# Performance work log

Measured on AMD Instinct MI355X. Metric: run time of the kernel, lower is better.

Reference implementation:

```python
import jax, jax.numpy as jnp
import numpy as np
from jax import lax

B, N, D, S, K = 8, 4096, 61, 1024, 32
MLP = (64, 64, 128)
WN = (3, 8, 8, 16)  # WeightNet: 3 -> 8 -> 8 -> 16
EPS = 1e-5


def _gather(p, idx):
    # p: [B, N, C], idx: [B, ...] -> [B, ..., C]
    return jax.vmap(lambda pb, ib: pb[ib])(p, idx)


def _fps(xyz, npoint, key):
    # farthest point sampling, xyz: [B, N, 3] -> idx [B, npoint]
    b, n, _ = xyz.shape
    start = jax.random.randint(key, (b,), 0, n)
    def step(carry, _):
        dmin, far = carry
        centroid = jnp.take_along_axis(xyz, far[:, None, None], axis=1)  # [B,1,3]
        d = jnp.sum((xyz - centroid) ** 2, -1)                            # [B,N]
        dmin = jnp.minimum(dmin, d)
        return (dmin, jnp.argmax(dmin, -1)), far
    _, idxs = lax.scan(step, (jnp.full((b, n), 1e10, xyz.dtype), start), None, length=npoint)
    return idxs.T  # [B, npoint]


def _sqdist(a, b):
    # a: [B,S,3], b: [B,N,3] -> [B,S,N]
    return (jnp.sum(a ** 2, -1)[:, :, None] + jnp.sum(b ** 2, -1)[:, None, :]
            - 2.0 * jnp.einsum('bsc,bnc->bsn', a, b))


def _bn_relu(x, g, be):
    # channels-last BN (training-mode batch stats, biased var) + ReLU
    axes = tuple(range(x.ndim - 1))
    m = x.mean(axes, keepdims=True)
    v = x.var(axes, keepdims=True)
    return jax.nn.relu(g * (x - m) * lax.rsqrt(v + EPS) + be)


def _forward(xyz, points, mlp_p, wn_p, lin_w, lin_b, bnl_g, bnl_b):
    xyz_t = xyz.transpose(0, 2, 1)    # [B,N,3]
    pts = points.transpose(0, 2, 1)   # [B,N,D]
    xyz_sg = lax.stop_gradient(xyz_t)  # index computations carry no grads (as in torch)
    fps_idx = _fps(xyz_sg, S, jax.random.key(42))  # [B,S]
    new_xyz = _gather(xyz_t, fps_idx)              # [B,S,3]
    idx = lax.top_k(-_sqdist(lax.stop_gradient(new_xyz), xyz_sg), K)[1]  # [B,S,K]
    g_norm = _gather(xyz_t, idx) - new_xyz[:, :, None, :]                # [B,S,K,3]
    feat = jnp.concatenate([g_norm, _gather(pts, idx)], -1)              # [B,S,K,3+D]
    for w, b, g, be in mlp_p:
        feat = _bn_relu(jnp.einsum('bskc,oc->bsko', feat, w) + b, g, be)
    wts = g_norm
    for w, b, g, be in wn_p:
        wts = _bn_relu(jnp.einsum('bskc,oc->bsko', wts, w) + b, g, be)   # [B,S,K,16]
    # [B,S,C,K] @ [B,S,K,16] -> [B,S,C,16] -> [B,S,C*16] (C-major flatten, as torch .view)
    agg = jnp.einsum('bskc,bskw->bscw', feat, wts).reshape(B, S, -1)
    out = agg @ lin_w.T + lin_b                                          # [B,S,128]
    m = out.mean((0, 1), keepdims=True)  # BatchNorm1d over batch and spatial
    v = out.var((0, 1), keepdims=True)
    out = jax.nn.relu(bnl_g * (out - m) * lax.rsqrt(v + EPS) + bnl_b)
    return new_xyz.transpose(0, 2, 1), out.transpose(0, 2, 1)  # [B,3,S], [B,128,S]


def setup_inputs() -> dict:
    key = jax.random.key(0)
    ks = iter(jax.random.split(key, 64))
    inp = {"xyz": jax.random.normal(next(ks), (B, 3, N), jnp.float32),
           "points": jax.random.normal(next(ks), (B, D, N), jnp.float32)}
    mlp_in = (3 + D,) + MLP[:-1]
    for i, (ci, co) in enumerate(zip(mlp_in, MLP)):
        inp[f"mlp_w{i}"] = jax.random.normal(next(ks), (co, ci), jnp.float32) / np.float32(np.sqrt(ci))
        inp[f"mlp_b{i}"] = jnp.zeros((co,), jnp.float32)
        inp[f"mlp_g{i}"] = jnp.ones((co,), jnp.float32)
        inp[f"mlp_be{i}"] = jnp.zeros((co,), jnp.float32)
    for i, (ci, co) in enumerate(zip(WN[:-1], WN[1:])):
        inp[f"wn_w{i}"] = jax.random.normal(next(ks), (co, ci), jnp.float32) / np.float32(np.sqrt(ci))
        inp[f"wn_b{i}"] = jnp.zeros((co,), jnp.float32)
        inp[f"wn_g{i}"] = jnp.ones((co,), jnp.float32)
        inp[f"wn_be{i}"] = jnp.zeros((co,), jnp.float32)
    fin = 16 * MLP[-1]
    inp["lin_w"] = jax.random.normal(next(ks), (MLP[-1], fin), jnp.float32) / np.float32(np.sqrt(fin))
    inp["lin_b"] = jnp.zeros((MLP[-1],), jnp.float32)
    inp["bnl_g"] = jnp.ones((MLP[-1],), jnp.float32)
    inp["bnl_b"] = jnp.zeros((MLP[-1],), jnp.float32)
    return inp


def reference(xyz, points, mlp_w0, mlp_b0, mlp_g0, mlp_be0, mlp_w1, mlp_b1, mlp_g1, mlp_be1, mlp_w2, mlp_b2, mlp_g2, mlp_be2, wn_w0, wn_b0, wn_g0, wn_be0, wn_w1, wn_b1, wn_g1, wn_be1, wn_w2, wn_b2, wn_g2, wn_be2, lin_w, lin_b, bnl_g, bnl_b):
    mlp_p = [(mlp_w0, mlp_b0, mlp_g0, mlp_be0),
             (mlp_w1, mlp_b1, mlp_g1, mlp_be1),
             (mlp_w2, mlp_b2, mlp_g2, mlp_be2)]
    wn_p = [(wn_w0, wn_b0, wn_g0, wn_be0),
            (wn_w1, wn_b1, wn_g1, wn_be1),
            (wn_w2, wn_b2, wn_g2, wn_be2)]
    return _forward(xyz, points, mlp_p, wn_p, lin_w, lin_b, bnl_g, bnl_b)
```

## Files before the change

kernel.cpp:

```cpp
#include <hip/hip_runtime.h>
#include <cstdint>
#include <cstddef>


constexpr int B_ = 8, N_ = 4096, D_ = 61, S_ = 1024, K_ = 32;
constexpr int P_ = B_ * S_ * K_;
constexpr int BS_ = B_ * S_;

constexpr size_t OFF_STATS  = 0;
constexpr size_t OFF_NEWXYZ = 8192;
constexpr size_t OFF_KNN    = 106496;
constexpr size_t OFF_PT     = 1155072;
constexpr size_t OFF_Y01    = 9543680;
constexpr size_t OFF_Y2     = 76652544;
constexpr size_t OFF_W01    = 210870272;
constexpr size_t OFF_W2B    = 219258880;
constexpr size_t OFF_OUTPRE = OFF_W01;

static inline uint32_t rotl32(uint32_t x, int r){ return (x << r) | (x >> (32 - r)); }
static void tf2x32(uint32_t k0, uint32_t k1, uint32_t x0, uint32_t x1,
                   uint32_t* o0, uint32_t* o1){
  uint32_t ks[3] = {k0, k1, k0 ^ k1 ^ 0x1BD11BDAu};
  x0 += ks[0]; x1 += ks[1];
  const int RA[4] = {13,15,26,6}, RB[4] = {17,29,16,24};
  for (int i = 0; i < 5; ++i){
    const int* R = (i & 1) ? RB : RA;
    for (int j = 0; j < 4; ++j){ x0 += x1; x1 = rotl32(x1, R[j]); x1 ^= x0; }
    x0 += ks[(i+1)%3]; x1 += ks[(i+2)%3] + (uint32_t)(i+1);
  }
  *o0 = x0; *o1 = x1;
}
struct StartIdx { int v[8]; };
static StartIdx compute_starts(){
  uint32_t ka, kb;
  tf2x32(0u, 42u, 0u, 1u, &ka, &kb);
  StartIdx s;
  for (int i = 0; i < 8; ++i){
    uint32_t b1, b2;
    tf2x32(ka, kb, 0u, (uint32_t)i, &b1, &b2);
    s.v[i] = (int)((b1 ^ b2) & 4095u);
  }
  return s;
}

template<int C>
__device__ __forceinline__ float dpp_max_f32_step(float x){
  int t = __builtin_amdgcn_update_dpp(0, (int)__float_as_uint(x), C, 0xf, 0xf, true);
  return fmaxf(x, __uint_as_float((unsigned)t));
}
__device__ __forceinline__ float dpp_wave_max_f32(float x){
  x = dpp_max_f32_step<0x111>(x);
  x = dpp_max_f32_step<0x112>(x);
  x = dpp_max_f32_step<0x114>(x);
  x = dpp_max_f32_step<0x118>(x);
  x = dpp_max_f32_step<0x142>(x);
  x = dpp_max_f32_step<0x143>(x);
  return __uint_as_float((unsigned)__builtin_amdgcn_readlane((int)__float_as_uint(x), 63));
}
template<int C>
__device__ __forceinline__ unsigned dpp_min_u32_step(unsigned x){
  int t = __builtin_amdgcn_update_dpp(-1, (int)x, C, 0xf, 0xf, false);
  unsigned u = (unsigned)t;
  return u < x ? u : x;
}
__device__ __forceinline__ unsigned dpp_wave_min_u32(unsigned x){
  x = dpp_min_u32_step<0x111>(x);
  x = dpp_min_u32_step<0x112>(x);
  x = dpp_min_u32_step<0x114>(x);
  x = dpp_min_u32_step<0x118>(x);
  x = dpp_min_u32_step<0x142>(x);
  x = dpp_min_u32_step<0x143>(x);
  return (unsigned)__builtin_amdgcn_readlane((int)x, 63);
}
template<int C>
__device__ __forceinline__ unsigned long long dpp_min_u64_step(unsigned long long k){
  unsigned lo = (unsigned)k, hi = (unsigned)(k >> 32);
  unsigned olo = (unsigned)__builtin_amdgcn_update_dpp(-1, (int)lo, C, 0xf, 0xf, false);
  unsigned ohi = (unsigned)__builtin_amdgcn_update_dpp(-1, (int)hi, C, 0xf, 0xf, false);
  unsigned long long o = ((unsigned long long)ohi << 32) | olo;
  return o < k ? o : k;
}
__device__ __forceinline__ unsigned long long dpp_wave_min_u64(unsigned long long k){
  k = dpp_min_u64_step<0x111>(k);
  k = dpp_min_u64_step<0x112>(k);
  k = dpp_min_u64_step<0x114>(k);
  k = dpp_min_u64_step<0x118>(k);
  k = dpp_min_u64_step<0x142>(k);
  k = dpp_min_u64_step<0x143>(k);
  unsigned lo = (unsigned)__builtin_amdgcn_readlane((int)(unsigned)k, 63);
  unsigned hi = (unsigned)__builtin_amdgcn_readlane((int)(unsigned)(k >> 32), 63);
  return ((unsigned long long)hi << 32) | lo;
}
__device__ __forceinline__ unsigned ordf(float f){
  unsigned u = __float_as_uint(f);
  return u ^ (unsigned)(((int)u >> 31) | 0x80000000);
}

__global__ __launch_bounds__(64) void tr_kernel(const float* __restrict__ pts,
                                                float* __restrict__ pT){
  __shared__ float tile[61][65];
  const int b = blockIdx.x >> 6;
  const int n0 = (blockIdx.x & 63) * 64;
  const int t = threadIdx.x;
  for (int d = 0; d < 61; ++d)
    tile[d][t] = pts[((size_t)b*61 + d)*N_ + n0 + t];
  __syncthreads();
  for (int r = 0; r < 64; ++r)
    pT[((size_t)b*N_ + n0 + r)*64 + t] = (t < 61) ? tile[t][r] : 0.f;
}

#define REP8(M) M(0) M(1) M(2) M(3) M(4) M(5) M(6) M(7)

__global__ __launch_bounds__(512, 1) void fps_kernel(const float* __restrict__ xyz,
                                                     StartIdx st,
                                                     float* __restrict__ new_xyz,
                                                     float* __restrict__ out_xyz){
  const int b = blockIdx.x, tid = threadIdx.x;
  const int lane = tid & 63, wv = tid >> 6;
  const float* xb = xyz + (size_t)b*3*N_;
  __shared__ float4 pts4[N_];
  __shared__ unsigned long long slots[2][8];

#define LOADP(i) \
  float px##i = xb[tid + 512*(i)]; \
  float py##i = xb[N_ + tid + 512*(i)]; \
  float pz##i = xb[2*N_ + tid + 512*(i)]; \
  float dm##i = 1e10f; \
  pts4[tid + 512*(i)] = make_float4(px##i, py##i, pz##i, 0.f);
  REP8(LOADP)
#undef LOADP
  __syncthreads();

  const int start = st.v[b];
  float4 c4 = pts4[start];
  float cx = c4.x, cy = c4.y, cz = c4.z;

  int par = 0;
  for (int s = 0; s < S_; ++s){
    if (tid == 0){
      new_xyz[((size_t)b*S_ + s)*3 + 0] = cx;
      new_xyz[((size_t)b*S_ + s)*3 + 1] = cy;
      new_xyz[((size_t)b*S_ + s)*3 + 2] = cz;
      out_xyz[(size_t)b*3*S_ + s]        = cx;
      out_xyz[(size_t)b*3*S_ + S_ + s]   = cy;
      out_xyz[(size_t)b*3*S_ + 2*S_ + s] = cz;
    }
#define UPD(i) { \
      float dx = __fsub_rn(px##i, cx), dy = __fsub_rn(py##i, cy), dz = __fsub_rn(pz##i, cz); \
      float d  = __fadd_rn(__fadd_rn(__fmul_rn(dx,dx), __fmul_rn(dy,dy)), __fmul_rn(dz,dz)); \
      dm##i = fminf(dm##i, d); }
    REP8(UPD)
#undef UPD
    float m01 = fmaxf(dm0, dm1), m23 = fmaxf(dm2, dm3);
    float m45 = fmaxf(dm4, dm5), m67 = fmaxf(dm6, dm7);
    float lmax = fmaxf(fmaxf(m01, m23), fmaxf(m45, m67));
    float wmax = dpp_wave_max_f32(lmax);
    unsigned cand = 0xFFFFFFFFu;
#define CAND(i) cand = (dm##i == wmax) ? (unsigned)(tid + 512*(i)) : cand;
    CAND(7) CAND(6) CAND(5) CAND(4) CAND(3) CAND(2) CAND(1) CAND(0)
#undef CAND
    unsigned widx = dpp_wave_min_u32(cand);
    if (lane == 63)
      slots[par][wv] = ((unsigned long long)__float_as_uint(wmax) << 32)
                     | (unsigned long long)(unsigned)(~widx);
    __syncthreads();
    unsigned long long bk = slots[par][0];
    { unsigned long long v1 = slots[par][1]; if (v1 > bk) bk = v1;
      unsigned long long v2 = slots[par][2]; if (v2 > bk) bk = v2;
      unsigned long long v3 = slots[par][3]; if (v3 > bk) bk = v3;
      unsigned long long v4 = slots[par][4]; if (v4 > bk) bk = v4;
      unsigned long long v5 = slots[par][5]; if (v5 > bk) bk = v5;
      unsigned long long v6 = slots[par][6]; if (v6 > bk) bk = v6;
      unsigned long long v7 = slots[par][7]; if (v7 > bk) bk = v7; }
    const int winner = (int)(~(unsigned)bk) & (N_ - 1);
    float4 w4 = pts4[winner];
    cx = w4.x; cy = w4.y; cz = w4.z;
    par ^= 1;
  }
}
#undef REP8

__global__ __launch_bounds__(256) void knn_kernel(const float* __restrict__ xyz,
                                                  const float* __restrict__ nxyz,
                                                  int* __restrict__ knn_idx){
  __shared__ float dist[4][4096];
  const int wv = threadIdx.x >> 6, lane = threadIdx.x & 63;
  const int q = blockIdx.x*4 + wv;
  const int b = q >> 10;
  const float* xb = xyz + (size_t)b*3*N_;
  const float ax = nxyz[(size_t)q*3], ay = nxyz[(size_t)q*3+1], az = nxyz[(size_t)q*3+2];
  const float sa = __fadd_rn(__fadd_rn(__fmul_rn(ax,ax), __fmul_rn(ay,ay)), __fmul_rn(az,az));
  float* dw = dist[wv];
  unsigned long long kk = ~0ull;
  for (int i = 0; i < 64; ++i){
    int n = i*64 + lane;
    float x = xb[n], y = xb[N_+n], z = xb[2*N_+n];
    float sb  = __fadd_rn(__fadd_rn(__fmul_rn(x,x), __fmul_rn(y,y)), __fmul_rn(z,z));
    float dot = __fadd_rn(__fadd_rn(__fmul_rn(ax,x), __fmul_rn(ay,y)), __fmul_rn(az,z));
    float d   = __fsub_rn(__fadd_rn(sa, sb), __fmul_rn(2.f, dot));
    dw[i*64 + ((lane + i) & 63)] = d;
    unsigned long long key = ((unsigned long long)ordf(d) << 32) | (unsigned)n;
    if (key < kk) kk = key;
  }
  __syncthreads();
  int myout = 0;
  for (int r = 0; r < 32; ++r){
    unsigned long long g = dpp_wave_min_u64(kk);
    const int gn = (int)(g & 0xFFFFFFFFull);
    if (lane == r) myout = gn;
    const int col = gn & 63, row = gn >> 6;
    const int a = lane*64 + ((col + lane) & 63);
    float v = dw[a];
    if (lane == row){ v = 3.4e38f; dw[a] = 3.4e38f; }
    unsigned long long nk = ((unsigned long long)ordf(v) << 32)
                          | (unsigned)(lane*64 + col);
    nk = dpp_wave_min_u64(nk);
    if (lane == col) kk = nk;
  }
  if (lane < 32) knn_idx[(size_t)q*32 + lane] = myout;
}

__global__ __launch_bounds__(256, 2) void m0_kernel(const float* __restrict__ pT,
                                                    const float* __restrict__ xyz,
                                                    const float* __restrict__ nxyz,
                                                    const int* __restrict__ knn_idx,
                                                    const float* __restrict__ w,
                                                    const float* __restrict__ bias,
                                                    float* __restrict__ y){
  __shared__ float Wt[4096]; __shared__ float bb[64];
  for (int t = threadIdx.x; t < 4096; t += 256){ int o = t >> 6, c = t & 63; Wt[c*64+o] = w[o*64+c]; }
  if (threadIdx.x < 64) bb[threadIdx.x] = bias[threadIdx.x];
  __syncthreads();
  const int p = blockIdx.x*256 + threadIdx.x;
  const int b = p >> 15, s = (p & 32767) >> 5;
  const int n = knn_idx[p];
  float in[64];
  {
    const float* xb = xyz + (size_t)b*3*N_;
    const int q = (b << 10) + s;
    in[0] = xb[n]       - nxyz[(size_t)q*3];
    in[1] = xb[N_+n]    - nxyz[(size_t)q*3+1];
    in[2] = xb[2*N_+n]  - nxyz[(size_t)q*3+2];
    const float* pr = pT + ((size_t)b*N_ + n)*64;
#pragma unroll
    for (int d = 0; d < 60; d += 4){
      float4 v = *reinterpret_cast<const float4*>(&pr[d]);
      in[3+d] = v.x; in[4+d] = v.y; in[5+d] = v.z; in[6+d] = v.w;
    }
    in[63] = pr[60];
  }
  float acc[64];
#pragma unroll
  for (int o = 0; o < 64; ++o) acc[o] = bb[o];
#pragma unroll
  for (int c = 0; c < 64; ++c){
    float x = in[c];
#pragma unroll
    for (int o = 0; o < 64; o += 4){
      float4 w4 = *reinterpret_cast<const float4*>(&Wt[c*64+o]);
      acc[o]   += x*w4.x; acc[o+1] += x*w4.y; acc[o+2] += x*w4.z; acc[o+3] += x*w4.w;
    }
  }
#pragma unroll
  for (int o = 0; o < 64; ++o) y[(size_t)o*P_ + p] = acc[o];
}

__global__ __launch_bounds__(256) void stats_kernel(const float* __restrict__ y,
                                                    double* __restrict__ st, int C){
  const int c = blockIdx.x % C, chunk = blockIdx.x / C;
  const float4* row4 = reinterpret_cast<const float4*>(y + (size_t)c*P_ + (size_t)chunk*32768);
  double s = 0.0, q = 0.0;
  for (int i = threadIdx.x; i < 8192; i += 256){
    float4 v = row4[i];
    s += (double)v.x + (double)v.y + (double)v.z + (double)v.w;
    q += (double)v.x*v.x + (double)v.y*v.y + (double)v.z*v.z + (double)v.w*v.w;
  }
  __shared__ double ss[256], qq[256];
  ss[threadIdx.x] = s; qq[threadIdx.x] = q; __syncthreads();
  for (int w = 128; w >= 1; w >>= 1){
    if (threadIdx.x < w){ ss[threadIdx.x] += ss[threadIdx.x+w]; qq[threadIdx.x] += qq[threadIdx.x+w]; }
    __syncthreads();
  }
  if (threadIdx.x == 0){ atomicAdd(&st[c*2], ss[0]); atomicAdd(&st[c*2+1], qq[0]); }
}

__device__ __forceinline__ void bn_coeff(const double* st, const float* g, const float* be,
                                         int c, double cnt, float* sc, float* sh){
  double mean = st[c*2] / cnt;
  double var  = st[c*2+1] / cnt - mean*mean;
  double scale = (double)g[c] / sqrt(var + 1e-5);
  *sc = (float)scale; *sh = (float)((double)be[c] - mean*scale);
}

__global__ __launch_bounds__(256, 2) void m1_kernel(float* __restrict__ y,
                                                    const float* __restrict__ w,
                                                    const float* __restrict__ bias,
                                                    const double* __restrict__ st,
                                                    const float* __restrict__ g,
                                                    const float* __restrict__ be){
  __shared__ float Wt[4096]; __shared__ float bb[64], sc[64], sh[64];
  for (int t = threadIdx.x; t < 4096; t += 256){ int o = t >> 6, c = t & 63; Wt[c*64+o] = w[o*64+c]; }
  if (threadIdx.x < 64){
    bn_coeff(st, g, be, threadIdx.x, (double)P_, &sc[threadIdx.x], &sh[threadIdx.x]);
    bb[threadIdx.x] = bias[threadIdx.x];
  }
  __syncthreads();
  const int p = blockIdx.x*256 + threadIdx.x;
  float in[64];
#pragma unroll
  for (int c = 0; c < 64; ++c){
    float x = y[(size_t)c*P_ + p];
    in[c] = fmaxf(0.f, fmaf(x, sc[c], sh[c]));
  }
  float acc[64];
#pragma unroll
  for (int o = 0; o < 64; ++o) acc[o] = bb[o];
#pragma unroll
  for (int c = 0; c < 64; ++c){
    float x = in[c];
#pragma unroll
    for (int o = 0; o < 64; o += 4){
      float4 w4 = *reinterpret_cast<const float4*>(&Wt[c*64+o]);
      acc[o]   += x*w4.x; acc[o+1] += x*w4.y; acc[o+2] += x*w4.z; acc[o+3] += x*w4.w;
    }
  }
#pragma unroll
  for (int o = 0; o < 64; ++o) y[(size_t)o*P_ + p] = acc[o];
}

__global__ __launch_bounds__(256, 2) void m2_kernel(const float* __restrict__ y1,
                                                    float* __restrict__ y2,
                                                    const float* __restrict__ w,
                                                    const float* __restrict__ bias,
                                                    const double* __restrict__ st,
                                                    const float* __restrict__ g,
                                                    const float* __restrict__ be){
  __shared__ float Wt[4096]; __shared__ float bb[64], sc[64], sh[64];
  const int half = blockIdx.y;
  for (int t = threadIdx.x; t < 4096; t += 256){
    int o = t >> 6, c = t & 63;
    Wt[c*64+o] = w[(size_t)(half*64+o)*64 + c];
  }
  if (threadIdx.x < 64){
    bn_coeff(st, g, be, threadIdx.x, (double)P_, &sc[threadIdx.x], &sh[threadIdx.x]);
    bb[threadIdx.x] = bias[half*64 + threadIdx.x];
  }
  __syncthreads();
  const int p = blockIdx.x*256 + threadIdx.x;
  float in[64];
#pragma unroll
  for (int c = 0; c < 64; ++c){
    float x = y1[(size_t)c*P_ + p];
    in[c] = fmaxf(0.f, fmaf(x, sc[c], sh[c]));
  }
  float acc[64];
#pragma unroll
  for (int o = 0; o < 64; ++o) acc[o] = bb[o];
#pragma unroll
  for (int c = 0; c < 64; ++c){
    float x = in[c];
#pragma unroll
    for (int o = 0; o < 64; o += 4){
      float4 w4 = *reinterpret_cast<const float4*>(&Wt[c*64+o]);
      acc[o]   += x*w4.x; acc[o+1] += x*w4.y; acc[o+2] += x*w4.z; acc[o+3] += x*w4.w;
    }
  }
#pragma unroll
  for (int o = 0; o < 64; ++o) y2[(size_t)(half*64+o)*P_ + p] = acc[o];
}

__global__ __launch_bounds__(256) void w0_kernel(const float* __restrict__ xyz,
                                                 const float* __restrict__ nxyz,
                                                 const int* __restrict__ knn_idx,
                                                 const float* __restrict__ w,
                                                 const float* __restrict__ bias,
                                                 float* __restrict__ wb){
  __shared__ float Wl[24], bb[8];
  if (threadIdx.x < 24) Wl[threadIdx.x] = w[threadIdx.x];
  if (threadIdx.x < 8)  bb[threadIdx.x] = bias[threadIdx.x];
  __syncthreads();
  const int p = blockIdx.x*256 + threadIdx.x;
  const int b = p >> 15, s = (p & 32767) >> 5;
  const int n = knn_idx[p];
  const float* xb = xyz + (size_t)b*3*N_;
  const int q = (b << 10) + s;
  float gx = xb[n]      - nxyz[(size_t)q*3];
  float gy = xb[N_+n]   - nxyz[(size_t)q*3+1];
  float gz = xb[2*N_+n] - nxyz[(size_t)q*3+2];
#pragma unroll
  for (int o = 0; o < 8; ++o){
    float a = bb[o] + gx*Wl[o*3] + gy*Wl[o*3+1] + gz*Wl[o*3+2];
    wb[(size_t)o*P_ + p] = a;
  }
}

__global__ __launch_bounds__(256) void w1_kernel(float* __restrict__ wb,
                                                 const float* __restrict__ w,
                                                 const float* __restrict__ bias,
                                                 const double* __restrict__ st,
                                                 const float* __restrict__ g,
                                                 const float* __restrict__ be){
  __shared__ float Wl[64], bb[8], sc[8], sh[8];
  if (threadIdx.x < 64) Wl[threadIdx.x] = w[threadIdx.x];
  if (threadIdx.x < 8){
    bn_coeff(st, g, be, threadIdx.x, (double)P_, &sc[threadIdx.x], &sh[threadIdx.x]);
    bb[threadIdx.x] = bias[threadIdx.x];
  }
  __syncthreads();
  const int p = blockIdx.x*256 + threadIdx.x;
  float in[8];
#pragma unroll
  for (int c = 0; c < 8; ++c){
    float x = wb[(size_t)c*P_ + p];
    in[c] = fmaxf(0.f, fmaf(x, sc[c], sh[c]));
  }
  float acc[8];
#pragma unroll
  for (int o = 0; o < 8; ++o){
    float a = bb[o];
#pragma unroll
    for (int c = 0; c < 8; ++c) a += in[c]*Wl[o*8+c];
    acc[o] = a;
  }
#pragma unroll
  for (int o = 0; o < 8; ++o) wb[(size_t)o*P_ + p] = acc[o];
}

__global__ __launch_bounds__(256) void w2_kernel(const float* __restrict__ wb,
                                                 float* __restrict__ wb2,
                                                 const float* __restrict__ w,
                                                 const float* __restrict__ bias,
                                                 const double* __restrict__ st,
                                                 const float* __restrict__ g,
                                                 const float* __restrict__ be){
  __shared__ float Wl[128], bb[16], sc[8], sh[8];
  if (threadIdx.x < 128) Wl[threadIdx.x] = w[threadIdx.x];
  if (threadIdx.x < 8)
    bn_coeff(st, g, be, threadIdx.x, (double)P_, &sc[threadIdx.x], &sh[threadIdx.x]);
  if (threadIdx.x < 16) bb[threadIdx.x] = bias[threadIdx.x];
  __syncthreads();
  const int p = blockIdx.x*256 + threadIdx.x;
  float in[8];
#pragma unroll
  for (int c = 0; c < 8; ++c){
    float x = wb[(size_t)c*P_ + p];
    in[c] = fmaxf(0.f, fmaf(x, sc[c], sh[c]));
  }
#pragma unroll
  for (int o = 0; o < 16; ++o){
    float a = bb[o];
#pragma unroll
    for (int c = 0; c < 8; ++c) a += in[c]*Wl[o*8+c];
    wb2[(size_t)o*P_ + p] = a;
  }
}

__global__ __launch_bounds__(256) void agg_kernel(const float* __restrict__ y2,
                                                  const float* __restrict__ wb2,
                                                  const double* __restrict__ st2,
                                                  const float* __restrict__ g2,
                                                  const float* __restrict__ be2,
                                                  const double* __restrict__ stw,
                                                  const float* __restrict__ gw,
                                                  const float* __restrict__ bew,
                                                  float* __restrict__ agg){
  __shared__ float f[32*132];
  __shared__ float wt[32*16];
  __shared__ float sc2[128], sh2[128], scw[16], shw[16];
  const int t = threadIdx.x;
  if (t < 128) bn_coeff(st2, g2, be2, t, (double)P_, &sc2[t], &sh2[t]);
  if (t < 16)  bn_coeff(stw, gw, bew, t, (double)P_, &scw[t], &shw[t]);
  __syncthreads();
  const int bs = blockIdx.x;
  const size_t p0 = (size_t)bs * 32;
  for (int e = t; e < 4096; e += 256){
    int c = e >> 5, k = e & 31;
    float x = y2[(size_t)c*P_ + p0 + k];
    f[k*132 + c] = fmaxf(0.f, fmaf(x, sc2[c], sh2[c]));
  }
  for (int e = t; e < 512; e += 256){
    int w = e >> 5, k = e & 31;
    float x = wb2[(size_t)w*P_ + p0 + k];
    wt[k*16 + w] = fmaxf(0.f, fmaf(x, scw[w], shw[w]));
  }
  __syncthreads();
  const int c = t >> 1, wp = (t & 1) * 8;
  float a0=0,a1=0,a2=0,a3=0,a4=0,a5=0,a6=0,a7=0;
#pragma unroll
  for (int k = 0; k < 32; ++k){
    float fv = f[k*132 + c];
    float4 u = *reinterpret_cast<const float4*>(&wt[k*16 + wp]);
    float4 v = *reinterpret_cast<const float4*>(&wt[k*16 + wp + 4]);
    a0 += fv*u.x; a1 += fv*u.y; a2 += fv*u.z; a3 += fv*u.w;
    a4 += fv*v.x; a5 += fv*v.y; a6 += fv*v.z; a7 += fv*v.w;
  }
  float* dst = agg + (size_t)bs*2048 + c*16 + wp;
  *reinterpret_cast<float4*>(dst)     = make_float4(a0,a1,a2,a3);
  *reinterpret_cast<float4*>(dst + 4) = make_float4(a4,a5,a6,a7);
}

__global__ __launch_bounds__(256) void lin_kernel(const float* __restrict__ agg,
                                                  const float* __restrict__ lw,
                                                  const float* __restrict__ lb,
                                                  float* __restrict__ outp){
  __shared__ float A[32*33];
  __shared__ float Wl[32*128];
  __shared__ float lbs[128];
  const int t = threadIdx.x;
  const int r0 = blockIdx.x * 32;
  if (t < 128) lbs[t] = lb[t];
  const int c_lane = t & 31, rg = t >> 5;
  float acc[4][4];
#pragma unroll
  for (int i = 0; i < 4; ++i)
#pragma unroll
    for (int j = 0; j < 4; ++j) acc[i][j] = 0.f;

  for (int kk0 = 0; kk0 < 2048; kk0 += 32){
    __syncthreads();
    {
      int r = t >> 3, kq = (t & 7) * 4;
      float4 v = *reinterpret_cast<const float4*>(&agg[(size_t)(r0 + r)*2048 + kk0 + kq]);
      A[r*33 + kq]   = v.x; A[r*33 + kq+1] = v.y; A[r*33 + kq+2] = v.z; A[r*33 + kq+3] = v.w;
    }
    {
#pragma unroll
      for (int u = 0; u < 4; ++u){
        int fid = t + 256*u;
        int o = fid >> 3, kq = (fid & 7) * 4;
        float4 v = *reinterpret_cast<const float4*>(&lw[(size_t)o*2048 + kk0 + kq]);
        Wl[(kq  )*128 + o] = v.x; Wl[(kq+1)*128 + o] = v.y;
        Wl[(kq+2)*128 + o] = v.z; Wl[(kq+3)*128 + o] = v.w;
      }
    }
    __syncthreads();
#pragma unroll 8
    for (int kk = 0; kk < 32; ++kk){
      float a0 = A[(rg*4+0)*33 + kk], a1 = A[(rg*4+1)*33 + kk],
            a2 = A[(rg*4+2)*33 + kk], a3 = A[(rg*4+3)*33 + kk];
#pragma unroll
      for (int j = 0; j < 4; ++j){
        float wv = Wl[kk*128 + c_lane + 32*j];
        acc[0][j] += a0*wv; acc[1][j] += a1*wv; acc[2][j] += a2*wv; acc[3][j] += a3*wv;
      }
    }
  }
  __syncthreads();
#pragma unroll
  for (int i = 0; i < 4; ++i)
#pragma unroll
    for (int j = 0; j < 4; ++j){
      int o = c_lane + 32*j;
      outp[(size_t)(r0 + rg*4 + i)*128 + o] = acc[i][j] + lbs[o];
    }
}

__global__ __launch_bounds__(128) void statsF_kernel(const float* __restrict__ outp,
                                                     double* __restrict__ st){
  const int c = threadIdx.x;
  const int r0 = blockIdx.x * 128;
  double s = 0.0, q = 0.0;
  for (int r = 0; r < 128; ++r){
    double v = outp[(size_t)(r0 + r)*128 + c];
    s += v; q += v*v;
  }
  atomicAdd(&st[c*2], s); atomicAdd(&st[c*2+1], q);
}

__global__ __launch_bounds__(256) void final_kernel(const float* __restrict__ outp,
                                                    const double* __restrict__ st,
                                                    const float* __restrict__ g,
                                                    const float* __restrict__ be,
                                                    float* __restrict__ out){
  const int gid = blockIdx.x*256 + threadIdx.x;
  const int s = gid & 1023, o = (gid >> 10) & 127, b = gid >> 17;
  float sc, sh;
  bn_coeff(st, g, be, o, (double)BS_, &sc, &sh);
  float x = outp[((size_t)(b << 10) + s)*128 + o];
  out[gid] = fmaxf(0.f, fmaf(x, sc, sh));
}

extern "C" void kernel_launch(void* const* d_in, const int* in_sizes, int n_in,
                              void* d_out, int out_size, void* d_ws, size_t ws_size,
                              hipStream_t stream){
  (void)in_sizes; (void)n_in; (void)out_size; (void)ws_size;
  const float* xyz    = (const float*)d_in[0];
  const float* points = (const float*)d_in[1];
  const float* mw0 = (const float*)d_in[2],  *mb0 = (const float*)d_in[3],
             * mg0 = (const float*)d_in[4],  *me0 = (const float*)d_in[5];
  const float* mw1 = (const float*)d_in[6],  *mb1 = (const float*)d_in[7],
             * mg1 = (const float*)d_in[8],  *me1 = (const float*)d_in[9];
  const float* mw2 = (const float*)d_in[10], *mb2 = (const float*)d_in[11],
             * mg2 = (const float*)d_in[12], *me2 = (const float*)d_in[13];
  const float* ww0 = (const float*)d_in[14], *wb0 = (const float*)d_in[15],
             * wg0 = (const float*)d_in[16], *we0 = (const float*)d_in[17];
  const float* ww1 = (const float*)d_in[18], *wb1 = (const float*)d_in[19],
             * wg1 = (const float*)d_in[20], *we1 = (const float*)d_in[21];
  const float* ww2 = (const float*)d_in[22], *wb2_ = (const float*)d_in[23],
             * wg2 = (const float*)d_in[24], *we2 = (const float*)d_in[25];
  const float* lw  = (const float*)d_in[26], *lb  = (const float*)d_in[27];
  const float* fg  = (const float*)d_in[28], *fb  = (const float*)d_in[29];

  char* ws = (char*)d_ws;
  double* ST0 = (double*)(ws + OFF_STATS);
  double* ST1 = (double*)(ws + OFF_STATS + 1024);
  double* ST2 = (double*)(ws + OFF_STATS + 2048);
  double* SW0 = (double*)(ws + OFF_STATS + 4096);
  double* SW1 = (double*)(ws + OFF_STATS + 4224);
  double* SW2 = (double*)(ws + OFF_STATS + 4352);
  double* STF = (double*)(ws + OFF_STATS + 4608);
  float* nxyz   = (float*)(ws + OFF_NEWXYZ);
  int*   knnidx = (int*)(ws + OFF_KNN);
  float* pT     = (float*)(ws + OFF_PT);
  float* y01    = (float*)(ws + OFF_Y01);
  float* y2     = (float*)(ws + OFF_Y2);
  float* w01    = (float*)(ws + OFF_W01);
  float* w2b    = (float*)(ws + OFF_W2B);
  float* aggbuf = (float*)(ws + OFF_Y01);
  float* outpre = (float*)(ws + OFF_OUTPRE);

  float* out_xyz  = (float*)d_out;
  float* out_feat = (float*)d_out + (size_t)B_*3*S_;

  hipMemsetAsync(ws + OFF_STATS, 0, 8192, stream);

  tr_kernel<<<dim3(B_*64), dim3(64), 0, stream>>>(points, pT);

  StartIdx st = compute_starts();
  fps_kernel<<<dim3(B_), dim3(512), 0, stream>>>(xyz, st, nxyz, out_xyz);

  knn_kernel<<<dim3(BS_/4), dim3(256), 0, stream>>>(xyz, nxyz, knnidx);

  m0_kernel<<<dim3(P_/256), dim3(256), 0, stream>>>(pT, xyz, nxyz, knnidx, mw0, mb0, y01);
  stats_kernel<<<dim3(64*8), dim3(256), 0, stream>>>(y01, ST0, 64);
  m1_kernel<<<dim3(P_/256), dim3(256), 0, stream>>>(y01, mw1, mb1, ST0, mg0, me0);
  stats_kernel<<<dim3(64*8), dim3(256), 0, stream>>>(y01, ST1, 64);
  m2_kernel<<<dim3(P_/256, 2), dim3(256), 0, stream>>>(y01, y2, mw2, mb2, ST1, mg1, me1);
  stats_kernel<<<dim3(128*8), dim3(256), 0, stream>>>(y2, ST2, 128);

  w0_kernel<<<dim3(P_/256), dim3(256), 0, stream>>>(xyz, nxyz, knnidx, ww0, wb0, w01);
  stats_kernel<<<dim3(8*8), dim3(256), 0, stream>>>(w01, SW0, 8);
  w1_kernel<<<dim3(P_/256), dim3(256), 0, stream>>>(w01, ww1, wb1, SW0, wg0, we0);
  stats_kernel<<<dim3(8*8), dim3(256), 0, stream>>>(w01, SW1, 8);
  w2_kernel<<<dim3(P_/256), dim3(256), 0, stream>>>(w01, w2b, ww2, wb2_, SW1, wg1, we1);
  stats_kernel<<<dim3(16*8), dim3(256), 0, stream>>>(w2b, SW2, 16);

  agg_kernel<<<dim3(BS_), dim3(256), 0, stream>>>(y2, w2b, ST2, mg2, me2, SW2, wg2, we2, aggbuf);
  lin_kernel<<<dim3(BS_/32), dim3(256), 0, stream>>>(aggbuf, lw, lb, outpre);
  statsF_kernel<<<dim3(BS_/128), dim3(128), 0, stream>>>(outpre, STF);
  final_kernel<<<dim3((B_*128*S_)/256), dim3(256), 0, stream>>>(outpre, STF, fg, fb, out_feat);
}
```

Measured before the change: 1.558 ms.

## Fuse BN stats into producer kernels, merge transpose into FPS, streamline FPS argmax

Removes the six standalone stats kernels by computing per-channel sum and sum-of-squares inside each producer kernel, using DPP row reductions, shared memory and double atomics. This saves re-reading the large activation buffers. The points transpose now runs as extra blocks of the FPS launch so it overlaps the single-block-per-batch FPS. FPS uses one packed 64-bit key max-reduction and defers writing the sampled coordinates until after the loop. The final kernel transposes through shared memory for coalesced stores. Stats are now accumulated in fp32 within a block before the double atomics, which slightly changes numerics, and the added atomics may contend.

```diff
diff --git a/kernel.cpp b/kernel.cpp
--- a/kernel.cpp
+++ b/kernel.cpp
@@ -44,33 +44,21 @@
 }
 
 template<int C>
-__device__ __forceinline__ float dpp_max_f32_step(float x){
-  int t = __builtin_amdgcn_update_dpp(0, (int)__float_as_uint(x), C, 0xf, 0xf, true);
-  return fmaxf(x, __uint_as_float((unsigned)t));
-}
-__device__ __forceinline__ float dpp_wave_max_f32(float x){
-  x = dpp_max_f32_step<0x111>(x);
-  x = dpp_max_f32_step<0x112>(x);
-  x = dpp_max_f32_step<0x114>(x);
-  x = dpp_max_f32_step<0x118>(x);
-  x = dpp_max_f32_step<0x142>(x);
-  x = dpp_max_f32_step<0x143>(x);
-  return __uint_as_float((unsigned)__builtin_amdgcn_readlane((int)__float_as_uint(x), 63));
-}
-template<int C>
-__device__ __forceinline__ unsigned dpp_min_u32_step(unsigned x){
-  int t = __builtin_amdgcn_update_dpp(-1, (int)x, C, 0xf, 0xf, false);
-  unsigned u = (unsigned)t;
-  return u < x ? u : x;
-}
-__device__ __forceinline__ unsigned dpp_wave_min_u32(unsigned x){
-  x = dpp_min_u32_step<0x111>(x);
-  x = dpp_min_u32_step<0x112>(x);
-  x = dpp_min_u32_step<0x114>(x);
-  x = dpp_min_u32_step<0x118>(x);
-  x = dpp_min_u32_step<0x142>(x);
-  x = dpp_min_u32_step<0x143>(x);
-  return (unsigned)__builtin_amdgcn_readlane((int)x, 63);
+__device__ __forceinline__ unsigned long long dpp_max_u64_step(unsigned long long k){
+  unsigned lo = (unsigned)k, hi = (unsigned)(k >> 32);
+  unsigned olo = (unsigned)__builtin_amdgcn_update_dpp(0, (int)lo, C, 0xf, 0xf, true);
+  unsigned ohi = (unsigned)__builtin_amdgcn_update_dpp(0, (int)hi, C, 0xf, 0xf, true);
+  unsigned long long o = ((unsigned long long)ohi << 32) | olo;
+  return o > k ? o : k;
+}
+__device__ __forceinline__ unsigned long long dpp_wave_max_u64(unsigned long long k){
+  k = dpp_max_u64_step<0x111>(k);
+  k = dpp_max_u64_step<0x112>(k);
+  k = dpp_max_u64_step<0x114>(k);
+  k = dpp_max_u64_step<0x118>(k);
+  k = dpp_max_u64_step<0x142>(k);
+  k = dpp_max_u64_step<0x143>(k);
+  return k;
 }
 template<int C>
 __device__ __forceinline__ unsigned long long dpp_min_u64_step(unsigned long long k){
@@ -91,78 +79,95 @@
   unsigned hi = (unsigned)__builtin_amdgcn_readlane((int)(unsigned)(k >> 32), 63);
   return ((unsigned long long)hi << 32) | lo;
 }
+template<int C>
+__device__ __forceinline__ float dpp_add_step(float x){
+  int t = __builtin_amdgcn_update_dpp(0, (int)__float_as_uint(x), C, 0xf, 0xf, true);
+  return x + __uint_as_float((unsigned)t);
+}
+__device__ __forceinline__ float dpp_row_sum16(float x){
+  x = dpp_add_step<0x111>(x);
+  x = dpp_add_step<0x112>(x);
+  x = dpp_add_step<0x114>(x);
+  x = dpp_add_step<0x118>(x);
+  return x;
+}
 __device__ __forceinline__ unsigned ordf(float f){
   unsigned u = __float_as_uint(f);
   return u ^ (unsigned)(((int)u >> 31) | 0x80000000);
 }
-
-__global__ __launch_bounds__(64) void tr_kernel(const float* __restrict__ pts,
-                                                float* __restrict__ pT){
-  __shared__ float tile[61][65];
-  const int b = blockIdx.x >> 6;
-  const int n0 = (blockIdx.x & 63) * 64;
-  const int t = threadIdx.x;
-  for (int d = 0; d < 61; ++d)
-    tile[d][t] = pts[((size_t)b*61 + d)*N_ + n0 + t];
-  __syncthreads();
-  for (int r = 0; r < 64; ++r)
-    pT[((size_t)b*N_ + n0 + r)*64 + t] = (t < 61) ? tile[t][r] : 0.f;
+__device__ __forceinline__ void atomAddD(double* p, double v){
+  __hip_atomic_fetch_add(p, v, __ATOMIC_RELAXED, __HIP_MEMORY_SCOPE_AGENT);
 }
 
 #define REP8(M) M(0) M(1) M(2) M(3) M(4) M(5) M(6) M(7)
 
-__global__ __launch_bounds__(512, 1) void fps_kernel(const float* __restrict__ xyz,
-                                                     StartIdx st,
-                                                     float* __restrict__ new_xyz,
-                                                     float* __restrict__ out_xyz){
-  const int b = blockIdx.x, tid = threadIdx.x;
+__global__ __launch_bounds__(512, 1) void fps_tr_kernel(const float* __restrict__ xyz,
+                                                        const float* __restrict__ pts,
+                                                        StartIdx st,
+                                                        float* __restrict__ new_xyz,
+                                                        float* __restrict__ out_xyz,
+                                                        float* __restrict__ pT){
+  __shared__ float4 pts4[N_];
+  __shared__ unsigned short win[S_];
+  __shared__ unsigned long long slots[2][8];
+  const int tid = threadIdx.x;
+
+  if (blockIdx.x >= 8){
+    float* tile = (float*)pts4;
+    const int tt = blockIdx.x - 8;
+    const int b = tt >> 6, n0 = (tt & 63) * 64;
+    for (int e = tid; e < 61*64; e += 512){
+      int d = e >> 6, c = e & 63;
+      tile[d*65 + c] = pts[((size_t)b*61 + d)*N_ + n0 + c];
+    }
+    __syncthreads();
+    for (int e = tid; e < 4096; e += 512){
+      int r = e >> 6, d = e & 63;
+      pT[((size_t)b*N_ + n0 + r)*64 + d] = (d < 61) ? tile[d*65 + r] : 0.f;
+    }
+    return;
+  }
+
+  const int b = blockIdx.x;
   const int lane = tid & 63, wv = tid >> 6;
   const float* xb = xyz + (size_t)b*3*N_;
-  __shared__ float4 pts4[N_];
-  __shared__ unsigned long long slots[2][8];
 
 #define LOADP(i) \
   float px##i = xb[tid + 512*(i)]; \
   float py##i = xb[N_ + tid + 512*(i)]; \
   float pz##i = xb[2*N_ + tid + 512*(i)]; \
   float dm##i = 1e10f; \
+  const unsigned kl##i = ~(unsigned)(tid + 512*(i)); \
   pts4[tid + 512*(i)] = make_float4(px##i, py##i, pz##i, 0.f);
   REP8(LOADP)
 #undef LOADP
   __syncthreads();
 
-  const int start = st.v[b];
-  float4 c4 = pts4[start];
+  int cur = st.v[b];
+  float4 c4 = pts4[cur];
   float cx = c4.x, cy = c4.y, cz = c4.z;
 
   int par = 0;
   for (int s = 0; s < S_; ++s){
-    if (tid == 0){
-      new_xyz[((size_t)b*S_ + s)*3 + 0] = cx;
-      new_xyz[((size_t)b*S_ + s)*3 + 1] = cy;
-      new_xyz[((size_t)b*S_ + s)*3 + 2] = cz;
-      out_xyz[(size_t)b*3*S_ + s]        = cx;
-      out_xyz[(size_t)b*3*S_ + S_ + s]   = cy;
-      out_xyz[(size_t)b*3*S_ + 2*S_ + s] = cz;
-    }
-#define UPD(i) { \
+    if (tid == 0) win[s] = (unsigned short)cur;
+    if (s == S_ - 1) break;
+#define UPD(i) \
+    unsigned long long key##i; { \
       float dx = __fsub_rn(px##i, cx), dy = __fsub_rn(py##i, cy), dz = __fsub_rn(pz##i, cz); \
       float d  = __fadd_rn(__fadd_rn(__fmul_rn(dx,dx), __fmul_rn(dy,dy)), __fmul_rn(dz,dz)); \
-      dm##i = fminf(dm##i, d); }
+      dm##i = fminf(dm##i, d); \
+      key##i = ((unsigned long long)__float_as_uint(dm##i) << 32) | kl##i; }
     REP8(UPD)
 #undef UPD
-    float m01 = fmaxf(dm0, dm1), m23 = fmaxf(dm2, dm3);
-    float m45 = fmaxf(dm4, dm5), m67 = fmaxf(dm6, dm7);
-    float lmax = fmaxf(fmaxf(m01, m23), fmaxf(m45, m67));
-    float wmax = dpp_wave_max_f32(lmax);
-    unsigned cand = 0xFFFFFFFFu;
-#define CAND(i) cand = (dm##i == wmax) ? (unsigned)(tid + 512*(i)) : cand;
-    CAND(7) CAND(6) CAND(5) CAND(4) CAND(3) CAND(2) CAND(1) CAND(0)
-#undef CAND
-    unsigned widx = dpp_wave_min_u32(cand);
-    if (lane == 63)
-      slots[par][wv] = ((unsigned long long)__float_as_uint(wmax) << 32)
-                     | (unsigned long long)(unsigned)(~widx);
+    unsigned long long t0 = key0 > key1 ? key0 : key1;
+    unsigned long long t1 = key2 > key3 ? key2 : key3;
+    unsigned long long t2 = key4 > key5 ? key4 : key5;
+    unsigned long long t3 = key6 > key7 ? key6 : key7;
+    unsigned long long u0 = t0 > t1 ? t0 : t1;
+    unsigned long long u1 = t2 > t3 ? t2 : t3;
+    unsigned long long k  = u0 > u1 ? u0 : u1;
+    k = dpp_wave_max_u64(k);
+    if (lane == 63) slots[par][wv] = k;
     __syncthreads();
     unsigned long long bk = slots[par][0];
     { unsigned long long v1 = slots[par][1]; if (v1 > bk) bk = v1;
@@ -172,10 +177,20 @@
       unsigned long long v5 = slots[par][5]; if (v5 > bk) bk = v5;
       unsigned long long v6 = slots[par][6]; if (v6 > bk) bk = v6;
       unsigned long long v7 = slots[par][7]; if (v7 > bk) bk = v7; }
-    const int winner = (int)(~(unsigned)bk) & (N_ - 1);
-    float4 w4 = pts4[winner];
+    cur = (int)(~(unsigned)bk) & (N_ - 1);
+    float4 w4 = pts4[cur];
     cx = w4.x; cy = w4.y; cz = w4.z;
     par ^= 1;
+  }
+  __syncthreads();
+  for (int s2 = tid; s2 < S_; s2 += 512){
+    float4 p = pts4[win[s2]];
+    new_xyz[((size_t)b*S_ + s2)*3 + 0] = p.x;
+    new_xyz[((size_t)b*S_ + s2)*3 + 1] = p.y;
+    new_xyz[((size_t)b*S_ + s2)*3 + 2] = p.z;
+    out_xyz[(size_t)b*3*S_ + s2]        = p.x;
+    out_xyz[(size_t)b*3*S_ + S_ + s2]   = p.y;
+    out_xyz[(size_t)b*3*S_ + 2*S_ + s2] = p.z;
   }
 }
 #undef REP8
@@ -220,14 +235,51 @@
   if (lane < 32) knn_idx[(size_t)q*32 + lane] = myout;
 }
 
+__device__ __forceinline__ void bn_coeff(const double* st, const float* g, const float* be,
+                                         int c, double cnt, float* sc, float* sh){
+  double mean = st[c*2] / cnt;
+  double var  = st[c*2+1] / cnt - mean*mean;
+  double scale = (double)g[c] / sqrt(var + 1e-5);
+  *sc = (float)scale; *sh = (float)((double)be[c] - mean*scale);
+}
+
+#define STATS64(ACC_EXPR, ST, CH_OFF)                                          \
+  {                                                                            \
+    _Pragma("unroll")                                                          \
+    for (int o = 0; o < 64; ++o){                                              \
+      float v_ = (ACC_EXPR);                                                   \
+      float s1_ = dpp_row_sum16(v_);                                           \
+      float q1_ = dpp_row_sum16(v_*v_);                                        \
+      if ((threadIdx.x & 15) == 15){                                           \
+        int rid_ = threadIdx.x >> 4;                                           \
+        redS[rid_][o] = s1_; redQ[rid_][o] = q1_;                              \
+      }                                                                        \
+    }                                                                          \
+    __syncthreads();                                                           \
+    if (threadIdx.x < 64){                                                     \
+      float s_ = 0.f;                                                          \
+      _Pragma("unroll")                                                        \
+      for (int r_ = 0; r_ < 16; ++r_) s_ += redS[r_][threadIdx.x];             \
+      atomAddD(&(ST)[((CH_OFF) + threadIdx.x)*2], (double)s_);                 \
+    } else if (threadIdx.x < 128){                                             \
+      int o_ = threadIdx.x - 64;                                               \
+      float s_ = 0.f;                                                          \
+      _Pragma("unroll")                                                        \
+      for (int r_ = 0; r_ < 16; ++r_) s_ += redQ[r_][o_];                      \
+      atomAddD(&(ST)[((CH_OFF) + o_)*2 + 1], (double)s_);                      \
+    }                                                                          \
+  }
+
 __global__ __launch_bounds__(256, 2) void m0_kernel(const float* __restrict__ pT,
                                                     const float* __restrict__ xyz,
                                                     const float* __restrict__ nxyz,
                                                     const int* __restrict__ knn_idx,
                                                     const float* __restrict__ w,
                                                     const float* __restrict__ bias,
-                                                    float* __restrict__ y){
+                                                    float* __restrict__ y,
+                                                    double* __restrict__ stout){
   __shared__ float Wt[4096]; __shared__ float bb[64];
+  __shared__ float redS[16][65], redQ[16][65];
   for (int t = threadIdx.x; t < 4096; t += 256){ int o = t >> 6, c = t & 63; Wt[c*64+o] = w[o*64+c]; }
   if (threadIdx.x < 64) bb[threadIdx.x] = bias[threadIdx.x];
   __syncthreads();
@@ -263,45 +315,21 @@
   }
 #pragma unroll
   for (int o = 0; o < 64; ++o) y[(size_t)o*P_ + p] = acc[o];
-}
-
-__global__ __launch_bounds__(256) void stats_kernel(const float* __restrict__ y,
-                                                    double* __restrict__ st, int C){
-  const int c = blockIdx.x % C, chunk = blockIdx.x / C;
-  const float4* row4 = reinterpret_cast<const float4*>(y + (size_t)c*P_ + (size_t)chunk*32768);
-  double s = 0.0, q = 0.0;
-  for (int i = threadIdx.x; i < 8192; i += 256){
-    float4 v = row4[i];
-    s += (double)v.x + (double)v.y + (double)v.z + (double)v.w;
-    q += (double)v.x*v.x + (double)v.y*v.y + (double)v.z*v.z + (double)v.w*v.w;
-  }
-  __shared__ double ss[256], qq[256];
-  ss[threadIdx.x] = s; qq[threadIdx.x] = q; __syncthreads();
-  for (int w = 128; w >= 1; w >>= 1){
-    if (threadIdx.x < w){ ss[threadIdx.x] += ss[threadIdx.x+w]; qq[threadIdx.x] += qq[threadIdx.x+w]; }
-    __syncthreads();
-  }
-  if (threadIdx.x == 0){ atomicAdd(&st[c*2], ss[0]); atomicAdd(&st[c*2+1], qq[0]); }
-}
-
-__device__ __forceinline__ void bn_coeff(const double* st, const float* g, const float* be,
-                                         int c, double cnt, float* sc, float* sh){
-  double mean = st[c*2] / cnt;
-  double var  = st[c*2+1] / cnt - mean*mean;
-  double scale = (double)g[c] / sqrt(var + 1e-5);
-  *sc = (float)scale; *sh = (float)((double)be[c] - mean*scale);
+  STATS64(acc[o], stout, 0)
 }
 
 __global__ __launch_bounds__(256, 2) void m1_kernel(float* __restrict__ y,
                                                     const float* __restrict__ w,
                                                     const float* __restrict__ bias,
-                                                    const double* __restrict__ st,
+                                                    const double* __restrict__ stin,
                                                     const float* __restrict__ g,
-                                                    const float* __restrict__ be){
+                                                    const float* __restrict__ be,
+                                                    double* __restrict__ stout){
   __shared__ float Wt[4096]; __shared__ float bb[64], sc[64], sh[64];
+  __shared__ float redS[16][65], redQ[16][65];
   for (int t = threadIdx.x; t < 4096; t += 256){ int o = t >> 6, c = t & 63; Wt[c*64+o] = w[o*64+c]; }
   if (threadIdx.x < 64){
-    bn_coeff(st, g, be, threadIdx.x, (double)P_, &sc[threadIdx.x], &sh[threadIdx.x]);
+    bn_coeff(stin, g, be, threadIdx.x, (double)P_, &sc[threadIdx.x], &sh[threadIdx.x]);
     bb[threadIdx.x] = bias[threadIdx.x];
   }
   __syncthreads();
@@ -326,23 +354,26 @@
   }
 #pragma unroll
   for (int o = 0; o < 64; ++o) y[(size_t)o*P_ + p] = acc[o];
+  STATS64(acc[o], stout, 0)
 }
 
 __global__ __launch_bounds__(256, 2) void m2_kernel(const float* __restrict__ y1,
                                                     float* __restrict__ y2,
                                                     const float* __restrict__ w,
                                                     const float* __restrict__ bias,
-                                                    const double* __restrict__ st,
+                                                    const double* __restrict__ stin,
                                                     const float* __restrict__ g,
-                                                    const float* __restrict__ be){
+                                                    const float* __restrict__ be,
+                                                    double* __restrict__ stout){
   __shared__ float Wt[4096]; __shared__ float bb[64], sc[64], sh[64];
+  __shared__ float redS[16][65], redQ[16][65];
   const int half = blockIdx.y;
   for (int t = threadIdx.x; t < 4096; t += 256){
     int o = t >> 6, c = t & 63;
     Wt[c*64+o] = w[(size_t)(half*64+o)*64 + c];
   }
   if (threadIdx.x < 64){
-    bn_coeff(st, g, be, threadIdx.x, (double)P_, &sc[threadIdx.x], &sh[threadIdx.x]);
+    bn_coeff(stin, g, be, threadIdx.x, (double)P_, &sc[threadIdx.x], &sh[threadIdx.x]);
     bb[threadIdx.x] = bias[half*64 + threadIdx.x];
   }
   __syncthreads();
@@ -367,6 +398,7 @@
   }
 #pragma unroll
   for (int o = 0; o < 64; ++o) y2[(size_t)(half*64+o)*P_ + p] = acc[o];
+  STATS64(acc[o], stout, half*64)
 }
 
 __global__ __launch_bounds__(256) void w0_kernel(const float* __restrict__ xyz,
@@ -374,8 +406,10 @@
                                                  const int* __restrict__ knn_idx,
                                                  const float* __restrict__ w,
                                                  const float* __restrict__ bias,
-                                                 float* __restrict__ wb){
+                                                 float* __restrict__ wb,
+                                                 double* __restrict__ stout){
   __shared__ float Wl[24], bb[8];
+  __shared__ float redS[16][9], redQ[16][9];
   if (threadIdx.x < 24) Wl[threadIdx.x] = w[threadIdx.x];
   if (threadIdx.x < 8)  bb[threadIdx.x] = bias[threadIdx.x];
   __syncthreads();
@@ -387,23 +421,45 @@
   float gx = xb[n]      - nxyz[(size_t)q*3];
   float gy = xb[N_+n]   - nxyz[(size_t)q*3+1];
   float gz = xb[2*N_+n] - nxyz[(size_t)q*3+2];
+  float a_[8];
 #pragma unroll
   for (int o = 0; o < 8; ++o){
-    float a = bb[o] + gx*Wl[o*3] + gy*Wl[o*3+1] + gz*Wl[o*3+2];
-    wb[(size_t)o*P_ + p] = a;
+    a_[o] = bb[o] + gx*Wl[o*3] + gy*Wl[o*3+1] + gz*Wl[o*3+2];
+    wb[(size_t)o*P_ + p] = a_[o];
+  }
+#pragma unroll
+  for (int o = 0; o < 8; ++o){
+    float s1 = dpp_row_sum16(a_[o]);
+    float q1 = dpp_row_sum16(a_[o]*a_[o]);
+    if ((threadIdx.x & 15) == 15){ int rid = threadIdx.x >> 4; redS[rid][o] = s1; redQ[rid][o] = q1; }
+  }
+  __syncthreads();
+  if (threadIdx.x < 8){
+    float s_ = 0.f;
+#pragma unroll
+    for (int r = 0; r < 16; ++r) s_ += redS[r][threadIdx.x];
+    atomAddD(&stout[threadIdx.x*2], (double)s_);
+  } else if (threadIdx.x < 16){
+    int o = threadIdx.x - 8;
+    float s_ = 0.f;
+#pragma unroll
+    for (int r = 0; r < 16; ++r) s_ += redQ[r][o];
+    atomAddD(&stout[o*2+1], (double)s_);
   }
 }
 
 __global__ __launch_bounds__(256) void w1_kernel(float* __restrict__ wb,
                                                  const float* __restrict__ w,
                                                  const float* __restrict__ bias,
-                                                 const double* __restrict__ st,
+                                                 const double* __restrict__ stin,
                                                  const float* __restrict__ g,
-                                                 const float* __restrict__ be){
+                                                 const float* __restrict__ be,
+                                                 double* __restrict__ stout){
   __shared__ float Wl[64], bb[8], sc[8], sh[8];
+  __shared__ float redS[16][9], redQ[16][9];
   if (threadIdx.x < 64) Wl[threadIdx.x] = w[threadIdx.x];
   if (threadIdx.x < 8){
-    bn_coeff(st, g, be, threadIdx.x, (double)P_, &sc[threadIdx.x], &sh[threadIdx.x]);
+    bn_coeff(stin, g, be, threadIdx.x, (double)P_, &sc[threadIdx.x], &sh[threadIdx.x]);
     bb[threadIdx.x] = bias[threadIdx.x];
   }
   __syncthreads();
@@ -424,19 +480,40 @@
   }
 #pragma unroll
   for (int o = 0; o < 8; ++o) wb[(size_t)o*P_ + p] = acc[o];
+#pragma unroll
+  for (int o = 0; o < 8; ++o){
+    float s1 = dpp_row_sum16(acc[o]);
+    float q1 = dpp_row_sum16(acc[o]*acc[o]);
+    if ((threadIdx.x & 15) == 15){ int rid = threadIdx.x >> 4; redS[rid][o] = s1; redQ[rid][o] = q1; }
+  }
+  __syncthreads();
+  if (threadIdx.x < 8){
+    float s_ = 0.f;
+#pragma unroll
+    for (int r = 0; r < 16; ++r) s_ += redS[r][threadIdx.x];
+    atomAddD(&stout[threadIdx.x*2], (double)s_);
+  } else if (threadIdx.x < 16){
+    int o = threadIdx.x - 8;
+    float s_ = 0.f;
+#pragma unroll
+    for (int r = 0; r < 16; ++r) s_ += redQ[r][o];
+    atomAddD(&stout[o*2+1], (double)s_);
+  }
 }
 
 __global__ __launch_bounds__(256) void w2_kernel(const float* __restrict__ wb,
                                                  float* __restrict__ wb2,
                                                  const float* __restrict__ w,
                                                  const float* __restrict__ bias,
-                                                 const double* __restrict__ st,
+                                                 const double* __restrict__ stin,
                                                  const float* __restrict__ g,
-                                                 const float* __restrict__ be){
+                                                 const float* __restrict__ be,
+                                                 double* __restrict__ stout){
   __shared__ float Wl[128], bb[16], sc[8], sh[8];
+  __shared__ float redS[16][17], redQ[16][17];
   if (threadIdx.x < 128) Wl[threadIdx.x] = w[threadIdx.x];
   if (threadIdx.x < 8)
-    bn_coeff(st, g, be, threadIdx.x, (double)P_, &sc[threadIdx.x], &sh[threadIdx.x]);
+    bn_coeff(stin, g, be, threadIdx.x, (double)P_, &sc[threadIdx.x], &sh[threadIdx.x]);
   if (threadIdx.x < 16) bb[threadIdx.x] = bias[threadIdx.x];
   __syncthreads();
   const int p = blockIdx.x*256 + threadIdx.x;
@@ -446,12 +523,33 @@
     float x = wb[(size_t)c*P_ + p];
     in[c] = fmaxf(0.f, fmaf(x, sc[c], sh[c]));
   }
+  float acc[16];
 #pragma unroll
   for (int o = 0; o < 16; ++o){
     float a = bb[o];
 #pragma unroll
     for (int c = 0; c < 8; ++c) a += in[c]*Wl[o*8+c];
+    acc[o] = a;
     wb2[(size_t)o*P_ + p] = a;
+  }
+#pragma unroll
+  for (int o = 0; o < 16; ++o){
+    float s1 = dpp_row_sum16(acc[o]);
+    float q1 = dpp_row_sum16(acc[o]*acc[o]);
+    if ((threadIdx.x & 15) == 15){ int rid = threadIdx.x >> 4; redS[rid][o] = s1; redQ[rid][o] = q1; }
+  }
+  __syncthreads();
+  if (threadIdx.x < 16){
+    float s_ = 0.f;
+#pragma unroll
+    for (int r = 0; r < 16; ++r) s_ += redS[r][threadIdx.x];
+    atomAddD(&stout[threadIdx.x*2], (double)s_);
+  } else if (threadIdx.x < 32){
+    int o = threadIdx.x - 16;
+    float s_ = 0.f;
+#pragma unroll
+    for (int r = 0; r < 16; ++r) s_ += redQ[r][o];
+    atomAddD(&stout[o*2+1], (double)s_);
   }
 }
 
@@ -564,7 +662,7 @@
     double v = outp[(size_t)(r0 + r)*128 + c];
     s += v; q += v*v;
   }
-  atomicAdd(&st[c*2], s); atomicAdd(&st[c*2+1], q);
+  atomAddD(&st[c*2], s); atomAddD(&st[c*2+1], q);
 }
 
 __global__ __launch_bounds__(256) void final_kernel(const float* __restrict__ outp,
@@ -572,12 +670,24 @@
                                                     const float* __restrict__ g,
                                                     const float* __restrict__ be,
                                                     float* __restrict__ out){
-  const int gid = blockIdx.x*256 + threadIdx.x;
-  const int s = gid & 1023, o = (gid >> 10) & 127, b = gid >> 17;
-  float sc, sh;
-  bn_coeff(st, g, be, o, (double)BS_, &sc, &sh);
-  float x = outp[((size_t)(b << 10) + s)*128 + o];
-  out[gid] = fmaxf(0.f, fmaf(x, sc, sh));
+  __shared__ float sc[128], sh[128];
+  __shared__ float tile[64][129];
+  const int t = threadIdx.x;
+  if (t < 128) bn_coeff(st, g, be, t, (double)BS_, &sc[t], &sh[t]);
+  const int bs0 = blockIdx.x * 64;
+  const int b = bs0 >> 10, s0 = bs0 & 1023;
+#pragma unroll
+  for (int e = t; e < 8192; e += 256){
+    int r = e >> 7, c = e & 127;
+    tile[r][c] = outp[(size_t)(bs0 + r)*128 + c];
+  }
+  __syncthreads();
+#pragma unroll
+  for (int e = t; e < 8192; e += 256){
+    int o = e >> 6, si = e & 63;
+    float x = tile[si][o];
+    out[(size_t)b*131072 + (size_t)o*1024 + s0 + si] = fmaxf(0.f, fmaf(x, sc[o], sh[o]));
+  }
 }
 
 extern "C" void kernel_launch(void* const* d_in, const int* in_sizes, int n_in,
@@ -624,29 +734,21 @@
 
   hipMemsetAsync(ws + OFF_STATS, 0, 8192, stream);
 
-  tr_kernel<<<dim3(B_*64), dim3(64), 0, stream>>>(points, pT);
-
   StartIdx st = compute_starts();
-  fps_kernel<<<dim3(B_), dim3(512), 0, stream>>>(xyz, st, nxyz, out_xyz);
+  fps_tr_kernel<<<dim3(8 + B_*64), dim3(512), 0, stream>>>(xyz, points, st, nxyz, out_xyz, pT);
 
   knn_kernel<<<dim3(BS_/4), dim3(256), 0, stream>>>(xyz, nxyz, knnidx);
 
-  m0_kernel<<<dim3(P_/256), dim3(256), 0, stream>>>(pT, xyz, nxyz, knnidx, mw0, mb0, y01);
-  stats_kernel<<<dim3(64*8), dim3(256), 0, stream>>>(y01, ST0, 64);
-  m1_kernel<<<dim3(P_/256), dim3(256), 0, stream>>>(y01, mw1, mb1, ST0, mg0, me0);
-  stats_kernel<<<dim3(64*8), dim3(256), 0, stream>>>(y01, ST1, 64);
-  m2_kernel<<<dim3(P_/256, 2), dim3(256), 0, stream>>>(y01, y2, mw2, mb2, ST1, mg1, me1);
-  stats_kernel<<<dim3(128*8), dim3(256), 0, stream>>>(y2, ST2, 128);
-
-  w0_kernel<<<dim3(P_/256), dim3(256), 0, stream>>>(xyz, nxyz, knnidx, ww0, wb0, w01);
-  stats_kernel<<<dim3(8*8), dim3(256), 0, stream>>>(w01, SW0, 8);
-  w1_kernel<<<dim3(P_/256), dim3(256), 0, stream>>>(w01, ww1, wb1, SW0, wg0, we0);
-  stats_kernel<<<dim3(8*8), dim3(256), 0, stream>>>(w01, SW1, 8);
-  w2_kernel<<<dim3(P_/256), dim3(256), 0, stream>>>(w01, w2b, ww2, wb2_, SW1, wg1, we1);
-  stats_kernel<<<dim3(16*8), dim3(256), 0, stream>>>(w2b, SW2, 16);
+  m0_kernel<<<dim3(P_/256), dim3(256), 0, stream>>>(pT, xyz, nxyz, knnidx, mw0, mb0, y01, ST0);
+  m1_kernel<<<dim3(P_/256), dim3(256), 0, stream>>>(y01, mw1, mb1, ST0, mg0, me0, ST1);
+  m2_kernel<<<dim3(P_/256, 2), dim3(256), 0, stream>>>(y01, y2, mw2, mb2, ST1, mg1, me1, ST2);
+
+  w0_kernel<<<dim3(P_/256), dim3(256), 0, stream>>>(xyz, nxyz, knnidx, ww0, wb0, w01, SW0);
+  w1_kernel<<<dim3(P_/256), dim3(256), 0, stream>>>(w01, ww1, wb1, SW0, wg0, we0, SW1);
+  w2_kernel<<<dim3(P_/256), dim3(256), 0, stream>>>(w01, w2b, ww2, wb2_, SW1, wg1, we1, SW2);
 
   agg_kernel<<<dim3(BS_), dim3(256), 0, stream>>>(y2, w2b, ST2, mg2, me2, SW2, wg2, we2, aggbuf);
   lin_kernel<<<dim3(BS_/32), dim3(256), 0, stream>>>(aggbuf, lw, lb, outpre);
   statsF_kernel<<<dim3(BS_/128), dim3(128), 0, stream>>>(outpre, STF);
-  final_kernel<<<dim3((B_*128*S_)/256), dim3(256), 0, stream>>>(outpre, STF, fg, fb, out_feat);
-}
+  final_kernel<<<dim3(BS_/64), dim3(256), 0, stream>>>(outpre, STF, fg, fb, out_feat);
+}
```

Measured after the change: 1.543 ms. Within noise of the previous version (-1.0%).
